# Performance work log

Hardware: AMD Instinct MI355X
Metric: run time of the kernel (lower is better)

## Reference

```python
import jax, jax.numpy as jnp
import numpy as np

D_MODEL = 1024
NUM_HEADS = 16
HEAD_DIM = D_MODEL // NUM_HEADS  # 64
D_FF = 4096
EPS = 1e-5


def layer_norm(x, gamma, beta):
    mu = jnp.mean(x, axis=-1, keepdims=True)
    var = jnp.mean((x - mu) ** 2, axis=-1, keepdims=True)
    return (x - mu) * jax.lax.rsqrt(var + EPS) * gamma + beta


def apply_rope(t):
    # t: [B, H, S, head_dim]; interleaved-pair rotation as in RoPE.apply_rope
    S, d = t.shape[-2], t.shape[-1]
    inv_freq = 1.0 / (10000.0 ** (jnp.arange(0, d, 2, dtype=jnp.float32) / d))  # [d/2]
    angles = jnp.arange(S, dtype=jnp.float32)[:, None] * inv_freq[None, :]      # [S, d/2]
    sin, cos = jnp.sin(angles), jnp.cos(angles)
    tp = t.reshape(*t.shape[:-1], d // 2, 2)  # pairs of adjacent elements
    t0, t1 = tp[..., 0], tp[..., 1]
    rot = jnp.stack([t0 * cos - t1 * sin, t0 * sin + t1 * cos], axis=-1)
    return rot.reshape(t.shape)


def setup_inputs() -> dict:
    key = jax.random.key(0)
    ks = jax.random.split(key, 18)
    s = 0.02
    d, f = D_MODEL, D_FF
    return {
        "x": jax.random.normal(ks[0], (2, 2048, d), dtype=jnp.float32),
        "Wq": jax.random.normal(ks[1], (d, d), dtype=jnp.float32) * s,
        "bq": jnp.zeros((d,), jnp.float32),
        "Wk": jax.random.normal(ks[2], (d, d), dtype=jnp.float32) * s,
        "bk": jnp.zeros((d,), jnp.float32),
        "Wv": jax.random.normal(ks[3], (d, d), dtype=jnp.float32) * s,
        "bv": jnp.zeros((d,), jnp.float32),
        "Wo": jax.random.normal(ks[4], (d, d), dtype=jnp.float32) * s,
        "bo": jnp.zeros((d,), jnp.float32),
        "W1": jax.random.normal(ks[5], (d, f), dtype=jnp.float32) * s,
        "b1": jnp.zeros((f,), jnp.float32),
        "W2": jax.random.normal(ks[6], (f, d), dtype=jnp.float32) * s,
        "b2": jnp.zeros((d,), jnp.float32),
        "g1": jnp.ones((d,), jnp.float32),
        "beta1": jnp.zeros((d,), jnp.float32),
        "g2": jnp.ones((d,), jnp.float32),
        "beta2": jnp.zeros((d,), jnp.float32),
    }


def reference(x, Wq, bq, Wk, bk, Wv, bv, Wo, bo, W1, b1, W2, b2, g1, beta1, g2, beta2):
    B, S, d = x.shape
    H, hd = NUM_HEADS, HEAD_DIM
    x_norm = layer_norm(x, g1, beta1)
    q = (x_norm @ Wq + bq).reshape(B, S, H, hd).transpose(0, 2, 1, 3)  # [B,H,S,hd]
    k = (x_norm @ Wk + bk).reshape(B, S, H, hd).transpose(0, 2, 1, 3)
    v = (x_norm @ Wv + bv).reshape(B, S, H, hd).transpose(0, 2, 1, 3)
    q = apply_rope(q)
    k = apply_rope(k)
    q = q * (1.0 / jnp.sqrt(jnp.float32(hd)))
    scores = jnp.einsum("bhqd,bhkd->bhqk", q, k)  # [B,H,S,S]
    attn = jax.nn.softmax(scores, axis=-1)
    out = jnp.einsum("bhqk,bhkd->bhqd", attn, v)
    out = out.transpose(0, 2, 1, 3).reshape(B, S, d)
    attn_out = out @ Wo + bo
    x = x + attn_out  # dropout p=0 (eval)
    x_norm2 = layer_norm(x, g2, beta2)
    ffn = jax.nn.relu(x_norm2 @ W1 + b1) @ W2 + b2
    return x + ffn
```

## Files before the change

### kernel.cpp

```cpp
#include <hip/hip_runtime.h>

typedef unsigned short bf16_t;
typedef short short8 __attribute__((ext_vector_type(8)));
typedef float f32x4 __attribute__((ext_vector_type(4)));

static __device__ __forceinline__ unsigned short f2bf(float f) {
  unsigned int u = __float_as_uint(f);
  unsigned int r = (u + 0x7FFFu + ((u >> 16) & 1u)) >> 16;
  return (unsigned short)r;
}
static __device__ __forceinline__ unsigned short f2bf_fast(float f) {
  return (unsigned short)((__float_as_uint(f) + 0x8000u) >> 16);
}
static __device__ __forceinline__ float bf2f(unsigned short u) {
  return __uint_as_float((unsigned int)u << 16);
}

__device__ __forceinline__ void gload_lds16(const void* g, void* l) {
  __builtin_amdgcn_global_load_lds((const __attribute__((address_space(1))) void*)g,
                                   (__attribute__((address_space(3))) void*)l,
                                   16, 0, 0);
}

__global__ __launch_bounds__(256) void prep_kernel(
    const float* __restrict__ Wq, const float* __restrict__ Wk,
    const float* __restrict__ Wv, const float* __restrict__ Wo,
    const float* __restrict__ W1, const float* __restrict__ W2,
    const float* __restrict__ x, const float* __restrict__ g1,
    const float* __restrict__ be1,
    bf16_t* __restrict__ WqkvT, bf16_t* __restrict__ W1T,
    bf16_t* __restrict__ W2T, bf16_t* __restrict__ xnb) {
  __shared__ float tile[32][33];
  const int bid = blockIdx.x;
  if (bid < 12288) {
    const float* src;
    bf16_t* dst;
    int rows, cols, bx, by;
    if (bid < 4096) {
      const int z = bid >> 10, r = bid & 1023;
      src = (z == 0) ? Wq : (z == 1) ? Wk : (z == 2) ? Wv : Wo;
      dst = WqkvT + (size_t)z * 1048576;
      rows = 1024; cols = 1024;
      bx = (r & 31) * 32; by = (r >> 5) * 32;
    } else if (bid < 8192) {
      const int r = bid - 4096;
      src = W1; dst = W1T; rows = 1024; cols = 4096;
      bx = (r & 127) * 32; by = (r >> 7) * 32;
    } else {
      const int r = bid - 8192;
      src = W2; dst = W2T; rows = 4096; cols = 1024;
      bx = (r & 31) * 32; by = (r >> 5) * 32;
    }
    const int tx = threadIdx.x & 31, ty = threadIdx.x >> 5;
#pragma unroll
    for (int i = 0; i < 32; i += 8)
      tile[ty + i][tx] = src[(size_t)(by + ty + i) * cols + (bx + tx)];
    __syncthreads();
#pragma unroll
    for (int i = 0; i < 32; i += 8)
      dst[(size_t)(bx + ty + i) * rows + (by + tx)] = f2bf(tile[tx][ty + i]);
  } else {
    const int row = bid - 12288;
    const int tid = threadIdx.x;
    const float4 v = reinterpret_cast<const float4*>(x + (size_t)row * 1024)[tid];
    float s = v.x + v.y + v.z + v.w;
    float ss = v.x * v.x + v.y * v.y + v.z * v.z + v.w * v.w;
#pragma unroll
    for (int off = 32; off; off >>= 1) {
      s += __shfl_xor(s, off, 64);
      ss += __shfl_xor(ss, off, 64);
    }
    float* red = &tile[0][0];
    const int wave = tid >> 6, lane = tid & 63;
    if (lane == 0) { red[wave] = s; red[4 + wave] = ss; }
    __syncthreads();
    const float mu = (red[0] + red[1] + red[2] + red[3]) * (1.f / 1024.f);
    const float ms = (red[4] + red[5] + red[6] + red[7]) * (1.f / 1024.f);
    const float rstd = rsqrtf(ms - mu * mu + 1e-5f);
    const float4 gg = reinterpret_cast<const float4*>(g1)[tid];
    const float4 bb = reinterpret_cast<const float4*>(be1)[tid];
    bf16_t* o = xnb + (size_t)row * 1024 + tid * 4;
    o[0] = f2bf((v.x - mu) * rstd * gg.x + bb.x);
    o[1] = f2bf((v.y - mu) * rstd * gg.y + bb.y);
    o[2] = f2bf((v.z - mu) * rstd * gg.z + bb.z);
    o[3] = f2bf((v.w - mu) * rstd * gg.w + bb.w);
  }
}

__global__ __launch_bounds__(256) void ln2_combine(const bf16_t* __restrict__ p,
                                                   const float* __restrict__ x,
                                                   const float* __restrict__ bo,
                                                   const float* __restrict__ g,
                                                   const float* __restrict__ be,
                                                   float* __restrict__ x2,
                                                   bf16_t* __restrict__ xn) {
  const int row = blockIdx.x;
  const int tid = threadIdx.x;
  const float4 xv = reinterpret_cast<const float4*>(x + (size_t)row * 1024)[tid];
  const float4 bb = reinterpret_cast<const float4*>(bo)[tid];
  float4 v = {bb.x + xv.x, bb.y + xv.y, bb.z + xv.z, bb.w + xv.w};
#pragma unroll
  for (int z = 0; z < 4; ++z) {
    const ushort4 a = reinterpret_cast<const ushort4*>(p + (size_t)z * 4194304 + (size_t)row * 1024)[tid];
    v.x += bf2f(a.x); v.y += bf2f(a.y); v.z += bf2f(a.z); v.w += bf2f(a.w);
  }
  reinterpret_cast<float4*>(x2 + (size_t)row * 1024)[tid] = v;
  float s = v.x + v.y + v.z + v.w;
  float ss = v.x * v.x + v.y * v.y + v.z * v.z + v.w * v.w;
#pragma unroll
  for (int off = 32; off; off >>= 1) {
    s += __shfl_xor(s, off, 64);
    ss += __shfl_xor(ss, off, 64);
  }
  __shared__ float red[8];
  const int wave = tid >> 6, lane = tid & 63;
  if (lane == 0) { red[wave] = s; red[4 + wave] = ss; }
  __syncthreads();
  const float mu = (red[0] + red[1] + red[2] + red[3]) * (1.f / 1024.f);
  const float ms = (red[4] + red[5] + red[6] + red[7]) * (1.f / 1024.f);
  const float rstd = rsqrtf(ms - mu * mu + 1e-5f);
  const float4 gg = reinterpret_cast<const float4*>(g)[tid];
  const float4 eb = reinterpret_cast<const float4*>(be)[tid];
  bf16_t* o = xn + (size_t)row * 1024 + tid * 4;
  o[0] = f2bf((v.x - mu) * rstd * gg.x + eb.x);
  o[1] = f2bf((v.y - mu) * rstd * gg.y + eb.y);
  o[2] = f2bf((v.z - mu) * rstd * gg.z + eb.z);
  o[3] = f2bf((v.w - mu) * rstd * gg.w + eb.w);
}

__global__ __launch_bounds__(256) void ffn_combine(const bf16_t* __restrict__ p0,
                                                   const bf16_t* __restrict__ p2,
                                                   const float* __restrict__ x2,
                                                   const float* __restrict__ b2,
                                                   float* __restrict__ out) {
  const int row = blockIdx.x;
  const int tid = threadIdx.x;
  const ushort4 a0 = reinterpret_cast<const ushort4*>(p0 + (size_t)row * 1024)[tid];
  const ushort4 a1 = reinterpret_cast<const ushort4*>(p0 + 4194304 + (size_t)row * 1024)[tid];
  const ushort4 a2 = reinterpret_cast<const ushort4*>(p2 + (size_t)row * 1024)[tid];
  const float4 xv = reinterpret_cast<const float4*>(x2 + (size_t)row * 1024)[tid];
  const float4 bb = reinterpret_cast<const float4*>(b2)[tid];
  float4 v;
  v.x = bf2f(a0.x) + bf2f(a1.x) + bf2f(a2.x) + bb.x + xv.x;
  v.y = bf2f(a0.y) + bf2f(a1.y) + bf2f(a2.y) + bb.y + xv.y;
  v.z = bf2f(a0.z) + bf2f(a1.z) + bf2f(a2.z) + bb.z + xv.z;
  v.w = bf2f(a0.w) + bf2f(a1.w) + bf2f(a2.w) + bb.w + xv.w;
  reinterpret_cast<float4*>(out + (size_t)row * 1024)[tid] = v;
}

__global__ __launch_bounds__(256) void rope_bf16(bf16_t* __restrict__ q,
                                                 bf16_t* __restrict__ k) {
  const int id = blockIdx.x * 256 + threadIdx.x;
  const int i = id & 31;
  const int s = (id >> 5) & 2047;
  const int bh = id >> 16;
  const float inv = exp2f((float)i * -0.41524101186f);
  float sn, cs;
  sincosf((float)s * inv, &sn, &cs);
  const size_t base = ((size_t)bh * 2048 + s) * 64 + 2 * i;
  unsigned int qp = *(unsigned int*)&q[base];
  unsigned int kp = *(unsigned int*)&k[base];
  const float q0 = bf2f(qp & 0xffff), q1 = bf2f(qp >> 16);
  const float k0 = bf2f(kp & 0xffff), k1 = bf2f(kp >> 16);
  const float qs = 0.18033688f;
  const unsigned int qo =
      (unsigned int)f2bf((q0 * cs - q1 * sn) * qs) |
      ((unsigned int)f2bf((q0 * sn + q1 * cs) * qs) << 16);
  const unsigned int ko =
      (unsigned int)f2bf(k0 * cs - k1 * sn) |
      ((unsigned int)f2bf(k0 * sn + k1 * cs) << 16);
  *(unsigned int*)&q[base] = qo;
  *(unsigned int*)&k[base] = ko;
}

__global__ __launch_bounds__(256) void vtrans(const bf16_t* __restrict__ v,
                                              bf16_t* __restrict__ vt) {
  __shared__ bf16_t tile[32][33];
  const int bh = blockIdx.x;
  const int s0 = blockIdx.y * 32;
  const int d0 = blockIdx.z * 32;
  const int tx = threadIdx.x & 31, ty = threadIdx.x >> 5;
  const size_t base = (size_t)bh * (2048 * 64);
#pragma unroll
  for (int i = 0; i < 32; i += 8)
    tile[ty + i][tx] = v[base + (size_t)(s0 + ty + i) * 64 + d0 + tx];
  __syncthreads();
#pragma unroll
  for (int i = 0; i < 32; i += 8)
    vt[base + (size_t)(d0 + ty + i) * 2048 + s0 + tx] = tile[tx][ty + i];
}

__global__ __launch_bounds__(256) void attn3(const bf16_t* __restrict__ qb,
                                             const bf16_t* __restrict__ kb,
                                             const bf16_t* __restrict__ vt,
                                             bf16_t* __restrict__ out) {
  const int bh = blockIdx.x;
  const int tid = threadIdx.x, wave = tid >> 6, lane = tid & 63;
  const int col = lane & 15, quad = lane >> 4;
  const int q0 = blockIdx.y * 128 + wave * 32;
  const size_t kvb = (size_t)bh * (2048 * 64);

  __shared__ __align__(16) bf16_t Ks[4096];
  __shared__ __align__(16) bf16_t Vs[4096];
  __shared__ __align__(16) bf16_t psw_all[4 * 32 * 72];
  bf16_t* psw = psw_all + wave * (32 * 72);

  short8 qf[2][2];
#pragma unroll
  for (int mi = 0; mi < 2; ++mi)
#pragma unroll
    for (int ks = 0; ks < 2; ++ks)
      qf[mi][ks] = *(const short8*)&qb[kvb + (size_t)(q0 + mi * 16 + col) * 64 + ks * 32 + quad * 8];

  f32x4 acc[2][4];
  float lsum[2][4];
#pragma unroll
  for (int mi = 0; mi < 2; ++mi)
#pragma unroll
    for (int n = 0; n < 4; ++n) acc[mi][n] = (f32x4){0.f, 0.f, 0.f, 0.f};
#pragma unroll
  for (int mi = 0; mi < 2; ++mi)
#pragma unroll
    for (int r = 0; r < 4; ++r) lsum[mi][r] = 0.f;

  const int swz = (col & 7);

  for (int t = 0; t < 2048; t += 64) {
#pragma unroll
    for (int j = 0; j < 2; ++j) {
      const int s = wave * 128 + j * 64 + lane;
      const int r = s >> 3;
      const int c = (s & 7) ^ (r & 7);
      gload_lds16(kb + kvb + (size_t)(t + r) * 64 + c * 8, Ks + (size_t)(wave * 128 + j * 64) * 8);
      gload_lds16(vt + kvb + (size_t)r * 2048 + t + c * 8, Vs + (size_t)(wave * 128 + j * 64) * 8);
    }
    __syncthreads();
    f32x4 sc[2][4];
#pragma unroll
    for (int mi = 0; mi < 2; ++mi)
#pragma unroll
      for (int n = 0; n < 4; ++n) sc[mi][n] = (f32x4){0.f, 0.f, 0.f, 0.f};
#pragma unroll
    for (int ks = 0; ks < 2; ++ks) {
      short8 kf[4];
#pragma unroll
      for (int n = 0; n < 4; ++n) {
        const int R = n * 16 + col;
        const int C = (ks * 4 + quad) ^ swz;
        kf[n] = *(const short8*)&Ks[(size_t)(R * 8 + C) * 8];
      }
#pragma unroll
      for (int mi = 0; mi < 2; ++mi)
#pragma unroll
        for (int n = 0; n < 4; ++n)
          sc[mi][n] = __builtin_amdgcn_mfma_f32_16x16x32_bf16(qf[mi][ks], kf[n], sc[mi][n], 0, 0, 0);
    }
#pragma unroll
    for (int mi = 0; mi < 2; ++mi)
#pragma unroll
      for (int n = 0; n < 4; ++n)
#pragma unroll
        for (int r = 0; r < 4; ++r) {
          const float pv = exp2f(sc[mi][n][r]);
          lsum[mi][r] += pv;
          psw[(mi * 16 + quad * 4 + r) * 72 + n * 16 + col] = f2bf_fast(pv);
        }
    short8 pf[2][2];
#pragma unroll
    for (int mi = 0; mi < 2; ++mi)
#pragma unroll
      for (int ks = 0; ks < 2; ++ks)
        pf[mi][ks] = *(const short8*)&psw[(mi * 16 + col) * 72 + ks * 32 + quad * 8];
#pragma unroll
    for (int ks = 0; ks < 2; ++ks) {
      short8 vf[4];
#pragma unroll
      for (int n = 0; n < 4; ++n) {
        const int R = n * 16 + col;
        const int C = (ks * 4 + quad) ^ swz;
        vf[n] = *(const short8*)&Vs[(size_t)(R * 8 + C) * 8];
      }
#pragma unroll
      for (int mi = 0; mi < 2; ++mi)
#pragma unroll
        for (int n = 0; n < 4; ++n)
          acc[mi][n] = __builtin_amdgcn_mfma_f32_16x16x32_bf16(pf[mi][ks], vf[n], acc[mi][n], 0, 0, 0);
    }
    __syncthreads();
  }

  const int b = bh >> 4, h = bh & 15;
#pragma unroll
  for (int mi = 0; mi < 2; ++mi)
#pragma unroll
    for (int r = 0; r < 4; ++r) {
      float s = lsum[mi][r];
      s += __shfl_xor(s, 1, 64);
      s += __shfl_xor(s, 2, 64);
      s += __shfl_xor(s, 4, 64);
      s += __shfl_xor(s, 8, 64);
      const float rl = 1.f / s;
      const size_t ro = (size_t)(b * 2048 + q0 + mi * 16 + quad * 4 + r) * 1024 + h * 64;
#pragma unroll
      for (int n = 0; n < 4; ++n) out[ro + n * 16 + col] = f2bf(acc[mi][n][r] * rl);
    }
}

enum { MODE_QKV = 0, MODE_FF1 = 1, MODE_PART = 2 };

template <int MODE>
__global__ __launch_bounds__(256) void gemm_bt(
    const bf16_t* __restrict__ A, const bf16_t* __restrict__ BT,
    int M, int N, int K, int kspan,
    const float* __restrict__ bias0, const float* __restrict__ bias1,
    const float* __restrict__ bias2,
    bf16_t* __restrict__ ob0, bf16_t* __restrict__ ob1, bf16_t* __restrict__ ob2) {
  __shared__ __align__(16) char smem[34816];
  bf16_t* As = (bf16_t*)smem;
  bf16_t* Bs = (bf16_t*)(smem + 16384);
  const int tid = threadIdx.x;
  const int wave = tid >> 6, lane = tid & 63;
  const int row16 = lane & 15, quad = lane >> 4;
  const int m0 = blockIdx.x * 128, n0 = blockIdx.y * 128;
  const int wm = (wave & 1) << 6, wn = (wave >> 1) << 6;

  f32x4 acc[4][4];
#pragma unroll
  for (int i = 0; i < 4; ++i)
#pragma unroll
    for (int j = 0; j < 4; ++j) acc[i][j] = (f32x4){0.f, 0.f, 0.f, 0.f};

  const int kb = blockIdx.z * kspan;
  const int kend = (kb + kspan < K) ? kb + kspan : K;

  for (int k0 = kb; k0 < kend; k0 += 64) {
#pragma unroll
    for (int j = 0; j < 4; ++j) {
      const int s = j * 256 + tid;
      const int r = s >> 3;
      const int cg = ((s & 7) ^ (r & 7)) << 3;
      gload_lds16(A + (size_t)(m0 + r) * K + k0 + cg, As + (size_t)s * 8);
      gload_lds16(BT + (size_t)(n0 + r) * K + k0 + cg, Bs + (size_t)s * 8);
    }
    __syncthreads();
    const int sw = row16 & 7;
#pragma unroll
    for (int kk = 0; kk < 2; ++kk) {
      short8 af[4], bfr[4];
#pragma unroll
      for (int mi = 0; mi < 4; ++mi)
        af[mi] = *(const short8*)&As[(size_t)(wm + mi * 16 + row16) * 64 + (((kk << 2) | quad) ^ sw) * 8];
#pragma unroll
      for (int ni = 0; ni < 4; ++ni)
        bfr[ni] = *(const short8*)&Bs[(size_t)(wn + ni * 16 + row16) * 64 + (((kk << 2) | quad) ^ sw) * 8];
#pragma unroll
      for (int mi = 0; mi < 4; ++mi)
#pragma unroll
        for (int ni = 0; ni < 4; ++ni)
          acc[mi][ni] =
              __builtin_amdgcn_mfma_f32_16x16x32_bf16(af[mi], bfr[ni], acc[mi][ni], 0, 0, 0);
    }
    __syncthreads();
  }

  bf16_t* ct = (bf16_t*)smem;
#pragma unroll
  for (int mi = 0; mi < 4; ++mi)
#pragma unroll
    for (int ni = 0; ni < 4; ++ni) {
      const int gn = n0 + wn + ni * 16 + row16;
      float bsv = 0.f;
      if (MODE == MODE_QKV)
        bsv = (gn < 1024) ? bias0[gn] : (gn < 2048) ? bias1[gn - 1024] : bias2[gn - 2048];
      else if (MODE == MODE_FF1)
        bsv = bias0[gn];
#pragma unroll
      for (int r = 0; r < 4; ++r) {
        float c = acc[mi][ni][r] + bsv;
        if (MODE == MODE_FF1) c = fmaxf(c, 0.f);
        ct[(size_t)(wm + mi * 16 + quad * 4 + r) * 136 + wn + ni * 16 + row16] = f2bf(c);
      }
    }
  __syncthreads();
  const int lr0 = tid >> 4, lc = tid & 15;
#pragma unroll
  for (int i = 0; i < 8; ++i) {
    const int lr = i * 16 + lr0;
    const uint4 v = *(const uint4*)&ct[(size_t)lr * 136 + lc * 8];
    const int gm = m0 + lr;
    if (MODE == MODE_QKV) {
      const int nn = (n0 & 1023) + lc * 8;
      const int h = nn >> 6, d = nn & 63;
      const int b = gm >> 11, s = gm & 2047;
      bf16_t* dst = (n0 < 1024) ? ob0 : (n0 < 2048) ? ob1 : ob2;
      *(uint4*)&dst[(((size_t)b * 16 + h) * 2048 + s) * 64 + d] = v;
    } else if (MODE == MODE_FF1) {
      *(uint4*)&ob0[(size_t)gm * N + n0 + lc * 8] = v;
    } else {
      bf16_t* dst = (blockIdx.z == 2) ? ob1 : ob0 + (size_t)blockIdx.z * 4194304;
      *(uint4*)&dst[(size_t)gm * N + n0 + lc * 8] = v;
    }
  }
}

extern "C" void kernel_launch(void* const* d_in, const int* in_sizes, int n_in,
                              void* d_out, int out_size, void* d_ws, size_t ws_size,
                              hipStream_t stream) {
  const float* x = (const float*)d_in[0];
  const float* Wq = (const float*)d_in[1];
  const float* bq = (const float*)d_in[2];
  const float* Wk = (const float*)d_in[3];
  const float* bk = (const float*)d_in[4];
  const float* Wv = (const float*)d_in[5];
  const float* bv = (const float*)d_in[6];
  const float* Wo = (const float*)d_in[7];
  const float* bo = (const float*)d_in[8];
  const float* W1 = (const float*)d_in[9];
  const float* b1 = (const float*)d_in[10];
  const float* W2 = (const float*)d_in[11];
  const float* b2 = (const float*)d_in[12];
  const float* g1 = (const float*)d_in[13];
  const float* be1 = (const float*)d_in[14];
  const float* g2 = (const float*)d_in[15];
  const float* be2 = (const float*)d_in[16];
  float* out = (float*)d_out;

  char* ws = (char*)d_ws;
  size_t off = 0;
  auto alloc = [&](size_t bytes) {
    void* p = ws + off;
    off += (bytes + 255) & ~(size_t)255;
    return p;
  };
  bf16_t* WqkvT = (bf16_t*)alloc(3072ULL * 1024 * 2);
  bf16_t* WoT = (bf16_t*)alloc(1024ULL * 1024 * 2);
  bf16_t* W1T = (bf16_t*)alloc(4096ULL * 1024 * 2);
  bf16_t* W2T = (bf16_t*)alloc(1024ULL * 4096 * 2);
  bf16_t* xnb = (bf16_t*)alloc(4096ULL * 1024 * 2);
  bf16_t* qb = (bf16_t*)alloc(4194304ULL * 2);
  bf16_t* kb = (bf16_t*)alloc(4194304ULL * 2);
  bf16_t* vraw = (bf16_t*)alloc(4194304ULL * 2);
  bf16_t* vt = (bf16_t*)alloc(4194304ULL * 2);
  bf16_t* h1 = qb;
  bf16_t* x2p = qb;
  bf16_t* ffp = WqkvT;
  float* x2 = (float*)alloc(16777216ULL);

  prep_kernel<<<16384, 256, 0, stream>>>(Wq, Wk, Wv, Wo, W1, W2, x, g1, be1,
                                         WqkvT, W1T, W2T, xnb);

  gemm_bt<MODE_QKV><<<dim3(32, 24, 1), 256, 0, stream>>>(xnb, WqkvT, 4096, 3072, 1024, 1024,
                                                         bq, bk, bv, qb, kb, vraw);

  rope_bf16<<<8192, 256, 0, stream>>>(qb, kb);

  vtrans<<<dim3(32, 64, 2), 256, 0, stream>>>(vraw, vt);

  attn3<<<dim3(32, 16), 256, 0, stream>>>(qb, kb, vt, xnb);

  gemm_bt<MODE_PART><<<dim3(32, 8, 4), 256, 0, stream>>>(xnb, WoT, 4096, 1024, 1024, 256,
                                                         nullptr, nullptr, nullptr,
                                                         x2p, x2p + 2 * 4194304, nullptr);

  ln2_combine<<<4096, 256, 0, stream>>>(x2p, x, bo, g2, be2, x2, xnb);

  gemm_bt<MODE_FF1><<<dim3(32, 32, 1), 256, 0, stream>>>(xnb, W1T, 4096, 4096, 1024, 1024,
                                                         b1, nullptr, nullptr,
                                                         h1, nullptr, nullptr);

  gemm_bt<MODE_PART><<<dim3(32, 8, 3), 256, 0, stream>>>(h1, W2T, 4096, 1024, 4096, 1408,
                                                         nullptr, nullptr, nullptr,
                                                         ffp, xnb, nullptr);

  ffn_combine<<<4096, 256, 0, stream>>>(ffp, xnb, x2, b2, out);
}
```

Before: 366.4 us.

## Double-buffer K/V tiles in attention and merge rope with V transpose

The attention kernel now keeps two LDS buffers for K and V and issues the global-to-LDS loads for the next 64-key tile before computing on the current one, so load latency can overlap the MFMA work. The rope and V-transpose kernels are merged into one launch, with a branch on block index, to save a kernel launch. The cost is double the K/V LDS footprint, which may lower occupancy. The loop still ends with a single __syncthreads per iteration, and it is unclear whether the async LDS loads are waited on correctly before the next tile is read.

New measurement: 370.6 us. Within noise of the previous version (+1.2%).

```diff
diff --git a/kernel.cpp b/kernel.cpp
--- a/kernel.cpp
+++ b/kernel.cpp
@@ -148,46 +148,50 @@
   reinterpret_cast<float4*>(out + (size_t)row * 1024)[tid] = v;
 }
 
-__global__ __launch_bounds__(256) void rope_bf16(bf16_t* __restrict__ q,
-                                                 bf16_t* __restrict__ k) {
-  const int id = blockIdx.x * 256 + threadIdx.x;
-  const int i = id & 31;
-  const int s = (id >> 5) & 2047;
-  const int bh = id >> 16;
-  const float inv = exp2f((float)i * -0.41524101186f);
-  float sn, cs;
-  sincosf((float)s * inv, &sn, &cs);
-  const size_t base = ((size_t)bh * 2048 + s) * 64 + 2 * i;
-  unsigned int qp = *(unsigned int*)&q[base];
-  unsigned int kp = *(unsigned int*)&k[base];
-  const float q0 = bf2f(qp & 0xffff), q1 = bf2f(qp >> 16);
-  const float k0 = bf2f(kp & 0xffff), k1 = bf2f(kp >> 16);
-  const float qs = 0.18033688f;
-  const unsigned int qo =
-      (unsigned int)f2bf((q0 * cs - q1 * sn) * qs) |
-      ((unsigned int)f2bf((q0 * sn + q1 * cs) * qs) << 16);
-  const unsigned int ko =
-      (unsigned int)f2bf(k0 * cs - k1 * sn) |
-      ((unsigned int)f2bf(k0 * sn + k1 * cs) << 16);
-  *(unsigned int*)&q[base] = qo;
-  *(unsigned int*)&k[base] = ko;
-}
-
-__global__ __launch_bounds__(256) void vtrans(const bf16_t* __restrict__ v,
-                                              bf16_t* __restrict__ vt) {
-  __shared__ bf16_t tile[32][33];
-  const int bh = blockIdx.x;
-  const int s0 = blockIdx.y * 32;
-  const int d0 = blockIdx.z * 32;
-  const int tx = threadIdx.x & 31, ty = threadIdx.x >> 5;
-  const size_t base = (size_t)bh * (2048 * 64);
-#pragma unroll
-  for (int i = 0; i < 32; i += 8)
-    tile[ty + i][tx] = v[base + (size_t)(s0 + ty + i) * 64 + d0 + tx];
-  __syncthreads();
-#pragma unroll
-  for (int i = 0; i < 32; i += 8)
-    vt[base + (size_t)(d0 + ty + i) * 2048 + s0 + tx] = tile[tx][ty + i];
+__global__ __launch_bounds__(256) void rope_vtrans(bf16_t* __restrict__ q,
+                                                   bf16_t* __restrict__ k,
+                                                   const bf16_t* __restrict__ v,
+                                                   bf16_t* __restrict__ vt) {
+  const int bid = blockIdx.x;
+  if (bid < 8192) {
+    const int id = bid * 256 + threadIdx.x;
+    const int i = id & 31;
+    const int s = (id >> 5) & 2047;
+    const int bh = id >> 16;
+    const float inv = exp2f((float)i * -0.41524101186f);
+    float sn, cs;
+    sincosf((float)s * inv, &sn, &cs);
+    const size_t base = ((size_t)bh * 2048 + s) * 64 + 2 * i;
+    unsigned int qp = *(unsigned int*)&q[base];
+    unsigned int kp = *(unsigned int*)&k[base];
+    const float q0 = bf2f(qp & 0xffff), q1 = bf2f(qp >> 16);
+    const float k0 = bf2f(kp & 0xffff), k1 = bf2f(kp >> 16);
+    const float qs = 0.18033688f;
+    const unsigned int qo =
+        (unsigned int)f2bf((q0 * cs - q1 * sn) * qs) |
+        ((unsigned int)f2bf((q0 * sn + q1 * cs) * qs) << 16);
+    const unsigned int ko =
+        (unsigned int)f2bf(k0 * cs - k1 * sn) |
+        ((unsigned int)f2bf(k0 * sn + k1 * cs) << 16);
+    *(unsigned int*)&q[base] = qo;
+    *(unsigned int*)&k[base] = ko;
+  } else {
+    __shared__ bf16_t tile[32][33];
+    const int r = bid - 8192;
+    const int bh = r >> 7;
+    const int rem = r & 127;
+    const int s0 = (rem >> 1) * 32;
+    const int d0 = (rem & 1) * 32;
+    const int tx = threadIdx.x & 31, ty = threadIdx.x >> 5;
+    const size_t base = (size_t)bh * (2048 * 64);
+#pragma unroll
+    for (int i = 0; i < 32; i += 8)
+      tile[ty + i][tx] = v[base + (size_t)(s0 + ty + i) * 64 + d0 + tx];
+    __syncthreads();
+#pragma unroll
+    for (int i = 0; i < 32; i += 8)
+      vt[base + (size_t)(d0 + ty + i) * 2048 + s0 + tx] = tile[tx][ty + i];
+  }
 }
 
 __global__ __launch_bounds__(256) void attn3(const bf16_t* __restrict__ qb,
@@ -200,8 +204,8 @@
   const int q0 = blockIdx.y * 128 + wave * 32;
   const size_t kvb = (size_t)bh * (2048 * 64);
 
-  __shared__ __align__(16) bf16_t Ks[4096];
-  __shared__ __align__(16) bf16_t Vs[4096];
+  __shared__ __align__(16) bf16_t Ks[2][4096];
+  __shared__ __align__(16) bf16_t Vs[2][4096];
   __shared__ __align__(16) bf16_t psw_all[4 * 32 * 72];
   bf16_t* psw = psw_all + wave * (32 * 72);
 
@@ -224,17 +228,33 @@
     for (int r = 0; r < 4; ++r) lsum[mi][r] = 0.f;
 
   const int swz = (col & 7);
-
-  for (int t = 0; t < 2048; t += 64) {
-#pragma unroll
-    for (int j = 0; j < 2; ++j) {
-      const int s = wave * 128 + j * 64 + lane;
-      const int r = s >> 3;
-      const int c = (s & 7) ^ (r & 7);
-      gload_lds16(kb + kvb + (size_t)(t + r) * 64 + c * 8, Ks + (size_t)(wave * 128 + j * 64) * 8);
-      gload_lds16(vt + kvb + (size_t)r * 2048 + t + c * 8, Vs + (size_t)(wave * 128 + j * 64) * 8);
-    }
-    __syncthreads();
+  int src_r[2], src_c[2];
+#pragma unroll
+  for (int j = 0; j < 2; ++j) {
+    const int s = wave * 128 + j * 64 + lane;
+    src_r[j] = s >> 3;
+    src_c[j] = ((s & 7) ^ ((s >> 3) & 7)) << 3;
+  }
+
+#pragma unroll
+  for (int j = 0; j < 2; ++j) {
+    gload_lds16(kb + kvb + (size_t)src_r[j] * 64 + src_c[j], &Ks[0][(wave * 128 + j * 64) * 8]);
+    gload_lds16(vt + kvb + (size_t)src_r[j] * 2048 + src_c[j], &Vs[0][(wave * 128 + j * 64) * 8]);
+  }
+  __syncthreads();
+
+  for (int it = 0; it < 32; ++it) {
+    const int t = it * 64;
+    const int cur = it & 1, nxt = cur ^ 1;
+    if (it + 1 < 32) {
+#pragma unroll
+      for (int j = 0; j < 2; ++j) {
+        gload_lds16(kb + kvb + (size_t)(t + 64 + src_r[j]) * 64 + src_c[j],
+                    &Ks[nxt][(wave * 128 + j * 64) * 8]);
+        gload_lds16(vt + kvb + (size_t)src_r[j] * 2048 + t + 64 + src_c[j],
+                    &Vs[nxt][(wave * 128 + j * 64) * 8]);
+      }
+    }
     f32x4 sc[2][4];
 #pragma unroll
     for (int mi = 0; mi < 2; ++mi)
@@ -247,7 +267,7 @@
       for (int n = 0; n < 4; ++n) {
         const int R = n * 16 + col;
         const int C = (ks * 4 + quad) ^ swz;
-        kf[n] = *(const short8*)&Ks[(size_t)(R * 8 + C) * 8];
+        kf[n] = *(const short8*)&Ks[cur][(size_t)(R * 8 + C) * 8];
       }
 #pragma unroll
       for (int mi = 0; mi < 2; ++mi)
@@ -278,7 +298,7 @@
       for (int n = 0; n < 4; ++n) {
         const int R = n * 16 + col;
         const int C = (ks * 4 + quad) ^ swz;
-        vf[n] = *(const short8*)&Vs[(size_t)(R * 8 + C) * 8];
+        vf[n] = *(const short8*)&Vs[cur][(size_t)(R * 8 + C) * 8];
       }
 #pragma unroll
       for (int mi = 0; mi < 2; ++mi)
@@ -452,9 +472,7 @@
   gemm_bt<MODE_QKV><<<dim3(32, 24, 1), 256, 0, stream>>>(xnb, WqkvT, 4096, 3072, 1024, 1024,
                                                          bq, bk, bv, qb, kb, vraw);
 
-  rope_bf16<<<8192, 256, 0, stream>>>(qb, kb);
-
-  vtrans<<<dim3(32, 64, 2), 256, 0, stream>>>(vraw, vt);
+  rope_vtrans<<<12288, 256, 0, stream>>>(qb, kb, vraw, vt);
 
   attn3<<<dim3(32, 16), 256, 0, stream>>>(qb, kb, vt, xnb);
 
```

## Fuse V transpose into QKV GEMM epilogue and halve attention query tile

Applied to the files above, without the earlier changes.

The QKV GEMM epilogue now writes V blocks already transposed (head-major d×s) by transposing the tile in shared memory, so the separate vtrans kernel and its extra round trip through global memory are removed. Separately, each attention wave now handles 16 query rows instead of 32, which doubles the grid to 32×32 blocks. The smaller tile gives more blocks and lower register pressure, but K/V tiles are reloaded by twice as many blocks. The transposed epilogue writes may also be less coalesced.

Result: slower. 375.0 us (+2.4%).

```diff
diff --git a/kernel.cpp b/kernel.cpp
--- a/kernel.cpp
+++ b/kernel.cpp
@@ -173,23 +173,6 @@
   *(unsigned int*)&k[base] = ko;
 }
 
-__global__ __launch_bounds__(256) void vtrans(const bf16_t* __restrict__ v,
-                                              bf16_t* __restrict__ vt) {
-  __shared__ bf16_t tile[32][33];
-  const int bh = blockIdx.x;
-  const int s0 = blockIdx.y * 32;
-  const int d0 = blockIdx.z * 32;
-  const int tx = threadIdx.x & 31, ty = threadIdx.x >> 5;
-  const size_t base = (size_t)bh * (2048 * 64);
-#pragma unroll
-  for (int i = 0; i < 32; i += 8)
-    tile[ty + i][tx] = v[base + (size_t)(s0 + ty + i) * 64 + d0 + tx];
-  __syncthreads();
-#pragma unroll
-  for (int i = 0; i < 32; i += 8)
-    vt[base + (size_t)(d0 + ty + i) * 2048 + s0 + tx] = tile[tx][ty + i];
-}
-
 __global__ __launch_bounds__(256) void attn3(const bf16_t* __restrict__ qb,
                                              const bf16_t* __restrict__ kb,
                                              const bf16_t* __restrict__ vt,
@@ -197,31 +180,25 @@
   const int bh = blockIdx.x;
   const int tid = threadIdx.x, wave = tid >> 6, lane = tid & 63;
   const int col = lane & 15, quad = lane >> 4;
-  const int q0 = blockIdx.y * 128 + wave * 32;
+  const int q0 = blockIdx.y * 64 + wave * 16;
   const size_t kvb = (size_t)bh * (2048 * 64);
 
   __shared__ __align__(16) bf16_t Ks[4096];
   __shared__ __align__(16) bf16_t Vs[4096];
-  __shared__ __align__(16) bf16_t psw_all[4 * 32 * 72];
-  bf16_t* psw = psw_all + wave * (32 * 72);
-
-  short8 qf[2][2];
-#pragma unroll
-  for (int mi = 0; mi < 2; ++mi)
-#pragma unroll
-    for (int ks = 0; ks < 2; ++ks)
-      qf[mi][ks] = *(const short8*)&qb[kvb + (size_t)(q0 + mi * 16 + col) * 64 + ks * 32 + quad * 8];
-
-  f32x4 acc[2][4];
-  float lsum[2][4];
-#pragma unroll
-  for (int mi = 0; mi < 2; ++mi)
-#pragma unroll
-    for (int n = 0; n < 4; ++n) acc[mi][n] = (f32x4){0.f, 0.f, 0.f, 0.f};
-#pragma unroll
-  for (int mi = 0; mi < 2; ++mi)
-#pragma unroll
-    for (int r = 0; r < 4; ++r) lsum[mi][r] = 0.f;
+  __shared__ __align__(16) bf16_t psw_all[4 * 16 * 72];
+  bf16_t* psw = psw_all + wave * (16 * 72);
+
+  short8 qf[2];
+#pragma unroll
+  for (int ks = 0; ks < 2; ++ks)
+    qf[ks] = *(const short8*)&qb[kvb + (size_t)(q0 + col) * 64 + ks * 32 + quad * 8];
+
+  f32x4 acc[4];
+  float lsum[4];
+#pragma unroll
+  for (int n = 0; n < 4; ++n) acc[n] = (f32x4){0.f, 0.f, 0.f, 0.f};
+#pragma unroll
+  for (int r = 0; r < 4; ++r) lsum[r] = 0.f;
 
   const int swz = (col & 7);
 
@@ -235,11 +212,9 @@
       gload_lds16(vt + kvb + (size_t)r * 2048 + t + c * 8, Vs + (size_t)(wave * 128 + j * 64) * 8);
     }
     __syncthreads();
-    f32x4 sc[2][4];
-#pragma unroll
-    for (int mi = 0; mi < 2; ++mi)
-#pragma unroll
-      for (int n = 0; n < 4; ++n) sc[mi][n] = (f32x4){0.f, 0.f, 0.f, 0.f};
+    f32x4 sc[4];
+#pragma unroll
+    for (int n = 0; n < 4; ++n) sc[n] = (f32x4){0.f, 0.f, 0.f, 0.f};
 #pragma unroll
     for (int ks = 0; ks < 2; ++ks) {
       short8 kf[4];
@@ -250,27 +225,21 @@
         kf[n] = *(const short8*)&Ks[(size_t)(R * 8 + C) * 8];
       }
 #pragma unroll
-      for (int mi = 0; mi < 2; ++mi)
-#pragma unroll
-        for (int n = 0; n < 4; ++n)
-          sc[mi][n] = __builtin_amdgcn_mfma_f32_16x16x32_bf16(qf[mi][ks], kf[n], sc[mi][n], 0, 0, 0);
-    }
-#pragma unroll
-    for (int mi = 0; mi < 2; ++mi)
-#pragma unroll
       for (int n = 0; n < 4; ++n)
-#pragma unroll
-        for (int r = 0; r < 4; ++r) {
-          const float pv = exp2f(sc[mi][n][r]);
-          lsum[mi][r] += pv;
-          psw[(mi * 16 + quad * 4 + r) * 72 + n * 16 + col] = f2bf_fast(pv);
-        }
-    short8 pf[2][2];
-#pragma unroll
-    for (int mi = 0; mi < 2; ++mi)
-#pragma unroll
-      for (int ks = 0; ks < 2; ++ks)
-        pf[mi][ks] = *(const short8*)&psw[(mi * 16 + col) * 72 + ks * 32 + quad * 8];
+        sc[n] = __builtin_amdgcn_mfma_f32_16x16x32_bf16(qf[ks], kf[n], sc[n], 0, 0, 0);
+    }
+#pragma unroll
+    for (int n = 0; n < 4; ++n)
+#pragma unroll
+      for (int r = 0; r < 4; ++r) {
+        const float pv = exp2f(sc[n][r]);
+        lsum[r] += pv;
+        psw[(quad * 4 + r) * 72 + n * 16 + col] = f2bf_fast(pv);
+      }
+    short8 pf[2];
+#pragma unroll
+    for (int ks = 0; ks < 2; ++ks)
+      pf[ks] = *(const short8*)&psw[col * 72 + ks * 32 + quad * 8];
 #pragma unroll
     for (int ks = 0; ks < 2; ++ks) {
       short8 vf[4];
@@ -281,29 +250,25 @@
         vf[n] = *(const short8*)&Vs[(size_t)(R * 8 + C) * 8];
       }
 #pragma unroll
-      for (int mi = 0; mi < 2; ++mi)
-#pragma unroll
-        for (int n = 0; n < 4; ++n)
-          acc[mi][n] = __builtin_amdgcn_mfma_f32_16x16x32_bf16(pf[mi][ks], vf[n], acc[mi][n], 0, 0, 0);
+      for (int n = 0; n < 4; ++n)
+        acc[n] = __builtin_amdgcn_mfma_f32_16x16x32_bf16(pf[ks], vf[n], acc[n], 0, 0, 0);
     }
     __syncthreads();
   }
 
   const int b = bh >> 4, h = bh & 15;
 #pragma unroll
-  for (int mi = 0; mi < 2; ++mi)
-#pragma unroll
-    for (int r = 0; r < 4; ++r) {
-      float s = lsum[mi][r];
-      s += __shfl_xor(s, 1, 64);
-      s += __shfl_xor(s, 2, 64);
-      s += __shfl_xor(s, 4, 64);
-      s += __shfl_xor(s, 8, 64);
-      const float rl = 1.f / s;
-      const size_t ro = (size_t)(b * 2048 + q0 + mi * 16 + quad * 4 + r) * 1024 + h * 64;
-#pragma unroll
-      for (int n = 0; n < 4; ++n) out[ro + n * 16 + col] = f2bf(acc[mi][n][r] * rl);
-    }
+  for (int r = 0; r < 4; ++r) {
+    float s = lsum[r];
+    s += __shfl_xor(s, 1, 64);
+    s += __shfl_xor(s, 2, 64);
+    s += __shfl_xor(s, 4, 64);
+    s += __shfl_xor(s, 8, 64);
+    const float rl = 1.f / s;
+    const size_t ro = (size_t)(b * 2048 + q0 + quad * 4 + r) * 1024 + h * 64;
+#pragma unroll
+    for (int n = 0; n < 4; ++n) out[ro + n * 16 + col] = f2bf(acc[n][r] * rl);
+  }
 }
 
 enum { MODE_QKV = 0, MODE_FF1 = 1, MODE_PART = 2 };
@@ -363,6 +328,7 @@
     __syncthreads();
   }
 
+  const bool vblk = (MODE == MODE_QKV) && (n0 >= 2048);
   bf16_t* ct = (bf16_t*)smem;
 #pragma unroll
   for (int mi = 0; mi < 4; ++mi)
@@ -378,7 +344,12 @@
       for (int r = 0; r < 4; ++r) {
         float c = acc[mi][ni][r] + bsv;
         if (MODE == MODE_FF1) c = fmaxf(c, 0.f);
-        ct[(size_t)(wm + mi * 16 + quad * 4 + r) * 136 + wn + ni * 16 + row16] = f2bf(c);
+        const int mm = wm + mi * 16 + quad * 4 + r;
+        const int nn = wn + ni * 16 + row16;
+        if (vblk)
+          ct[(size_t)nn * 136 + mm] = f2bf(c);
+        else
+          ct[(size_t)mm * 136 + nn] = f2bf(c);
       }
     }
   __syncthreads();
@@ -387,18 +358,26 @@
   for (int i = 0; i < 8; ++i) {
     const int lr = i * 16 + lr0;
     const uint4 v = *(const uint4*)&ct[(size_t)lr * 136 + lc * 8];
-    const int gm = m0 + lr;
-    if (MODE == MODE_QKV) {
-      const int nn = (n0 & 1023) + lc * 8;
+    if (vblk) {
+      const int nn = (n0 - 2048) + lr;
       const int h = nn >> 6, d = nn & 63;
+      const int gm = m0 + lc * 8;
       const int b = gm >> 11, s = gm & 2047;
-      bf16_t* dst = (n0 < 1024) ? ob0 : (n0 < 2048) ? ob1 : ob2;
-      *(uint4*)&dst[(((size_t)b * 16 + h) * 2048 + s) * 64 + d] = v;
-    } else if (MODE == MODE_FF1) {
-      *(uint4*)&ob0[(size_t)gm * N + n0 + lc * 8] = v;
+      *(uint4*)&ob2[(((size_t)b * 16 + h) * 64 + d) * 2048 + s] = v;
     } else {
-      bf16_t* dst = (blockIdx.z == 2) ? ob1 : ob0 + (size_t)blockIdx.z * 4194304;
-      *(uint4*)&dst[(size_t)gm * N + n0 + lc * 8] = v;
+      const int gm = m0 + lr;
+      if (MODE == MODE_QKV) {
+        const int nn = (n0 & 1023) + lc * 8;
+        const int h = nn >> 6, d = nn & 63;
+        const int b = gm >> 11, s = gm & 2047;
+        bf16_t* dst = (n0 < 1024) ? ob0 : ob1;
+        *(uint4*)&dst[(((size_t)b * 16 + h) * 2048 + s) * 64 + d] = v;
+      } else if (MODE == MODE_FF1) {
+        *(uint4*)&ob0[(size_t)gm * N + n0 + lc * 8] = v;
+      } else {
+        bf16_t* dst = (blockIdx.z == 2) ? ob1 : ob0 + (size_t)blockIdx.z * 4194304;
+        *(uint4*)&dst[(size_t)gm * N + n0 + lc * 8] = v;
+      }
     }
   }
 }
@@ -439,8 +418,8 @@
   bf16_t* xnb = (bf16_t*)alloc(4096ULL * 1024 * 2);
   bf16_t* qb = (bf16_t*)alloc(4194304ULL * 2);
   bf16_t* kb = (bf16_t*)alloc(4194304ULL * 2);
-  bf16_t* vraw = (bf16_t*)alloc(4194304ULL * 2);
   bf16_t* vt = (bf16_t*)alloc(4194304ULL * 2);
+  (void)alloc(8ULL << 20);
   bf16_t* h1 = qb;
   bf16_t* x2p = qb;
   bf16_t* ffp = WqkvT;
@@ -450,13 +429,11 @@
                                          WqkvT, W1T, W2T, xnb);
 
   gemm_bt<MODE_QKV><<<dim3(32, 24, 1), 256, 0, stream>>>(xnb, WqkvT, 4096, 3072, 1024, 1024,
-                                                         bq, bk, bv, qb, kb, vraw);
+                                                         bq, bk, bv, qb, kb, vt);
 
   rope_bf16<<<8192, 256, 0, stream>>>(qb, kb);
 
-  vtrans<<<dim3(32, 64, 2), 256, 0, stream>>>(vraw, vt);
-
-  attn3<<<dim3(32, 16), 256, 0, stream>>>(qb, kb, vt, xnb);
+  attn3<<<dim3(32, 32), 256, 0, stream>>>(qb, kb, vt, xnb);
 
   gemm_bt<MODE_PART><<<dim3(32, 8, 4), 256, 0, stream>>>(xnb, WoT, 4096, 1024, 1024, 256,
                                                          nullptr, nullptr, nullptr,
```
